# Performance work log

Hardware: AMD Instinct MI355X
Metric: run time of the kernel (lower is better)

## Reference

```python
import jax, jax.numpy as jnp
import numpy as np
import math

HEADS = 16
D_MODEL = 1024
HEAD_DIM = D_MODEL // HEADS
B, S = 2, 2048


def setup_inputs() -> dict:
    key = jax.random.key(0)
    ks = jax.random.split(key, 12)
    sc = 1.0 / math.sqrt(D_MODEL)
    inp = {
        "query": jax.random.normal(ks[0], (B, S, D_MODEL), jnp.float32),
        "key_t": jax.random.normal(ks[1], (B, S, D_MODEL), jnp.float32),
        "value": jax.random.normal(ks[2], (B, S, D_MODEL), jnp.float32),
        "mask": jax.random.randint(ks[3], (B, 1, 1, S), 0, 2, jnp.int32),
        "Wq": jax.random.normal(ks[4], (D_MODEL, D_MODEL), jnp.float32) * sc,
        "bq": jnp.zeros((D_MODEL,), jnp.float32),
        "Wk": jax.random.normal(ks[5], (D_MODEL, D_MODEL), jnp.float32) * sc,
        "bk": jnp.zeros((D_MODEL,), jnp.float32),
        "Wv": jax.random.normal(ks[6], (D_MODEL, D_MODEL), jnp.float32) * sc,
        "bv": jnp.zeros((D_MODEL,), jnp.float32),
        "Wo": jax.random.normal(ks[7], (D_MODEL, D_MODEL), jnp.float32) * sc,
        "bo": jnp.zeros((D_MODEL,), jnp.float32),
    }
    return inp


def _split_heads(x):
    # [B, S, D] -> [B, H, S, Dh]
    b, s, _ = x.shape
    return x.reshape(b, s, HEADS, HEAD_DIM).transpose(0, 2, 1, 3)


def reference(query, key_t, value, mask, Wq, bq, Wk, bk, Wv, bv, Wo, bo):
    # Linear projections (torch Linear: x @ W.T + b)
    q = _split_heads(query @ Wq.T + bq)
    k = _split_heads(key_t @ Wk.T + bk)
    v = _split_heads(value @ Wv.T + bv)
    # Scaled dot-product attention; scale by sqrt(head_dim) = query.size(-1) after split
    scores = jnp.einsum("bhqd,bhkd->bhqk", q, k) / math.sqrt(HEAD_DIM)
    scores = jnp.where(mask == 0, jnp.float32(-1e9), scores)
    prob = jax.nn.softmax(scores, axis=-1)
    # dropout is identity at inference
    attn = jnp.einsum("bhqk,bhkd->bhqd", prob, v)
    # [B, H, S, Dh] -> [B, S, D]
    attn = attn.transpose(0, 2, 1, 3).reshape(query.shape[0], -1, D_MODEL)
    return attn @ Wo.T + bo
```

## Files before the change

kernel.cpp:

```cpp
#include <hip/hip_runtime.h>
#include <hip/hip_bf16.h>

typedef __bf16 bf16;
typedef __bf16 bf16x8 __attribute__((ext_vector_type(8)));
typedef __bf16 bf16x4 __attribute__((ext_vector_type(4)));
typedef float  f32x4  __attribute__((ext_vector_type(4)));
typedef float  f32x16 __attribute__((ext_vector_type(16)));

#define AS1 __attribute__((address_space(1)))
#define AS3 __attribute__((address_space(3)))

__device__ __forceinline__ void gload_lds16(const bf16* g, bf16* l) {
    __builtin_amdgcn_global_load_lds((const AS1 unsigned int*)g,
                                     (AS3 unsigned int*)l, 16, 0, 0);
}

__global__ __launch_bounds__(256) void cast7_k(
    const float* __restrict__ s0, const float* __restrict__ s1,
    const float* __restrict__ s2, const float* __restrict__ s3,
    const float* __restrict__ s4, const float* __restrict__ s5,
    const float* __restrict__ s6,
    bf16* __restrict__ d0, bf16* __restrict__ d1, bf16* __restrict__ d2,
    bf16* __restrict__ d3, bf16* __restrict__ d4, bf16* __restrict__ d5,
    bf16* __restrict__ d6, int n_big, int n_small) {
    int z = blockIdx.z;
    const float* s = (z == 0) ? s0 : (z == 1) ? s1 : (z == 2) ? s2
                   : (z == 3) ? s3 : (z == 4) ? s4 : (z == 5) ? s5 : s6;
    bf16* d = (z == 0) ? d0 : (z == 1) ? d1 : (z == 2) ? d2
            : (z == 3) ? d3 : (z == 4) ? d4 : (z == 5) ? d5 : d6;
    int n = (z < 3) ? n_big : n_small;
    int i = (blockIdx.x * 256 + threadIdx.x) * 8;
    if (i >= n) return;
    float4 a = *(const float4*)(s + i);
    float4 b = *(const float4*)(s + i + 4);
    bf16x8 o;
    o[0] = (bf16)a.x; o[1] = (bf16)a.y; o[2] = (bf16)a.z; o[3] = (bf16)a.w;
    o[4] = (bf16)b.x; o[5] = (bf16)b.y; o[6] = (bf16)b.z; o[7] = (bf16)b.w;
    *(bf16x8*)(d + i) = o;
}

__global__ __launch_bounds__(256) void mask_bias_k(
    const int* __restrict__ m, float* __restrict__ mb, int n) {
    int i = blockIdx.x * 256 + threadIdx.x;
    if (i < n) mb[i] = (m[i] == 0) ? -1.442695e9f : -17.3123405f;
}

template <typename OUT_T, bool TRANS>
__device__ __forceinline__ void gemm32_core(
    const bf16* __restrict__ A, const bf16* __restrict__ W,
    const float* __restrict__ bias, OUT_T* __restrict__ C,
    int M, int N, int K) {
    __shared__ bf16 Asm[128 * 64];
    __shared__ bf16 Bsm[128 * 64];
    const int lane = threadIdx.x & 63;
    const int w = threadIdx.x >> 6;
    const int l31 = lane & 31;
    const int h = lane >> 5;
    const int x7 = l31 & 7;
    const int m0 = blockIdx.x * 128;
    const int n0 = blockIdx.y * 128;
    const int srow = lane >> 3;
    const int scol = ((lane & 7) ^ srow) * 8;
    const int wm = (w & 1) * 64;
    const int wn = (w >> 1) * 64;

    f32x16 acc[2][2] = {};

    for (int k0 = 0; k0 < K; k0 += 64) {
#pragma unroll
        for (int c = 0; c < 4; ++c) {
            int r = w * 32 + c * 8;
            gload_lds16(A + (size_t)(m0 + r + srow) * K + k0 + scol, &Asm[r * 64]);
            gload_lds16(W + (size_t)(n0 + r + srow) * K + k0 + scol, &Bsm[r * 64]);
        }
        __syncthreads();
#pragma unroll
        for (int step = 0; step < 4; ++step) {
            bf16x8 af[2], bfv[2];
#pragma unroll
            for (int i = 0; i < 2; ++i)
                af[i] = *(const bf16x8*)&Asm[(wm + i * 32 + l31) * 64 +
                                             (((step * 2 + h) ^ x7) * 8)];
#pragma unroll
            for (int j = 0; j < 2; ++j)
                bfv[j] = *(const bf16x8*)&Bsm[(wn + j * 32 + l31) * 64 +
                                              (((step * 2 + h) ^ x7) * 8)];
#pragma unroll
            for (int i = 0; i < 2; ++i)
#pragma unroll
                for (int j = 0; j < 2; ++j)
                    acc[i][j] = TRANS
                        ? __builtin_amdgcn_mfma_f32_32x32x16_bf16(bfv[j], af[i],
                                                                  acc[i][j], 0, 0, 0)
                        : __builtin_amdgcn_mfma_f32_32x32x16_bf16(af[i], bfv[j],
                                                                  acc[i][j], 0, 0, 0);
        }
        __syncthreads();
    }
    if (!TRANS) {
#pragma unroll
        for (int i = 0; i < 2; ++i)
#pragma unroll
            for (int j = 0; j < 2; ++j) {
                int col = n0 + wn + j * 32 + l31;
                float bv = bias[col];
#pragma unroll
                for (int g = 0; g < 4; ++g)
#pragma unroll
                    for (int rr = 0; rr < 4; ++rr) {
                        int row = m0 + wm + i * 32 + rr + g * 8 + 4 * h;
                        C[(size_t)row * N + col] =
                            (OUT_T)(acc[i][j][g * 4 + rr] + bv);
                    }
            }
    } else {
#pragma unroll
        for (int i = 0; i < 2; ++i) {
            int s = m0 + wm + i * 32 + l31;
            int b = s >> 11;
            int sl = s & 2047;
            int sp = (sl & ~12) | ((sl & 4) << 1) | ((sl & 8) >> 1);
#pragma unroll
            for (int j = 0; j < 2; ++j)
#pragma unroll
                for (int g = 0; g < 4; ++g) {
                    float4 bv4 = *(const float4*)&bias[n0 + wn + j * 32 + g * 8 + 4 * h];
#pragma unroll
                    for (int rr = 0; rr < 4; ++rr) {
                        int n = n0 + wn + j * 32 + g * 8 + 4 * h + rr;
                        C[(size_t)(b * 1024 + n) * 2048 + sp] =
                            (OUT_T)(acc[i][j][g * 4 + rr] + (&bv4.x)[rr]);
                    }
                }
        }
    }
}

__global__ __launch_bounds__(256) void gemm_qkv(
    const bf16* __restrict__ qb, const bf16* __restrict__ kb, const bf16* __restrict__ vb,
    const bf16* __restrict__ Wq, const bf16* __restrict__ Wk, const bf16* __restrict__ Wv,
    const float* __restrict__ bq, const float* __restrict__ bk, const float* __restrict__ bv,
    bf16* __restrict__ Qp, bf16* __restrict__ Kp, bf16* __restrict__ VpT) {
    int z = blockIdx.z;
    if (z == 2) {
        gemm32_core<bf16, true>(vb, Wv, bv, VpT, 4096, 1024, 1024);
    } else {
        const bf16* A = (z == 0) ? qb : kb;
        const bf16* W = (z == 0) ? Wq : Wk;
        const float* bi = (z == 0) ? bq : bk;
        bf16* C = (z == 0) ? Qp : Kp;
        gemm32_core<bf16, false>(A, W, bi, C, 4096, 1024, 1024);
    }
}

__global__ __launch_bounds__(256) void gemm_out(
    const bf16* __restrict__ A, const bf16* __restrict__ W,
    const float* __restrict__ bias, float* __restrict__ C) {
    gemm32_core<float, false>(A, W, bias, C, 4096, 1024, 1024);
}

__global__ __launch_bounds__(256) void attn_k(
    const bf16* __restrict__ Qp, const bf16* __restrict__ Kp,
    const bf16* __restrict__ VpT, const float* __restrict__ mb,
    bf16* __restrict__ Ao) {
    __shared__ bf16 Ksm[64 * 64];
    __shared__ bf16 Vsm[64 * 64];
    const int q0 = blockIdx.x * 128;
    const int bh = blockIdx.y;
    const int b = bh >> 4, hh = bh & 15;
    const int lane = threadIdx.x & 63, w = threadIdx.x >> 6;
    const int l31 = lane & 31, h = lane >> 5;
    const int x7 = l31 & 7;
    const int srow = lane >> 3, scol = ((lane & 7) ^ srow) * 8;
    const float SC = 0.125f * 1.44269504f;

    const bf16* Qbase =
        Qp + (size_t)(b * 2048 + q0 + w * 32 + l31) * 1024 + hh * 64;
    bf16x8 qf[4];
#pragma unroll
    for (int step = 0; step < 4; ++step)
        qf[step] = *(const bf16x8*)(Qbase + step * 16 + h * 8);

    f32x16 o[2] = {};
    float lsum = 0.0f;

    const float* mbb = mb + b * 2048;
    const bf16* Kg = Kp + (size_t)(b * 2048) * 1024 + hh * 64;
    const bf16* Vg = VpT + (size_t)bh * 64 * 2048;

    for (int k0 = 0; k0 < 2048; k0 += 64) {
#pragma unroll
        for (int c = 0; c < 2; ++c) {
            int r = w * 16 + c * 8;
            gload_lds16(Kg + (size_t)(k0 + r + srow) * 1024 + scol, &Ksm[r * 64]);
            gload_lds16(Vg + (size_t)(r + srow) * 2048 + k0 + scol, &Vsm[r * 64]);
        }
        __syncthreads();

        bf16x8 pa[4];
#pragma unroll
        for (int kg = 0; kg < 2; ++kg) {
            f32x16 z = {};
#pragma unroll
            for (int step = 0; step < 4; ++step) {
                bf16x8 kf = *(const bf16x8*)&Ksm[(kg * 32 + l31) * 64 +
                                                 (((step * 2 + h) ^ x7) * 8)];
                z = __builtin_amdgcn_mfma_f32_32x32x16_bf16(kf, qf[step], z, 0, 0, 0);
            }
            float p[16];
#pragma unroll
            for (int g = 0; g < 4; ++g) {
                float4 bia = *(const float4*)&mbb[k0 + kg * 32 + g * 8 + 4 * h];
                p[g * 4 + 0] = __builtin_amdgcn_exp2f(fmaf(z[g * 4 + 0], SC, bia.x));
                p[g * 4 + 1] = __builtin_amdgcn_exp2f(fmaf(z[g * 4 + 1], SC, bia.y));
                p[g * 4 + 2] = __builtin_amdgcn_exp2f(fmaf(z[g * 4 + 2], SC, bia.z));
                p[g * 4 + 3] = __builtin_amdgcn_exp2f(fmaf(z[g * 4 + 3], SC, bia.w));
            }
#pragma unroll
            for (int t = 0; t < 16; ++t) lsum += p[t];
#pragma unroll
            for (int half = 0; half < 2; ++half) {
                bf16x8 pt;
#pragma unroll
                for (int j = 0; j < 8; ++j) pt[j] = (bf16)p[half * 8 + j];
                pa[kg * 2 + half] = pt;
            }
        }
#pragma unroll
        for (int t = 0; t < 2; ++t)
#pragma unroll
            for (int kk = 0; kk < 4; ++kk) {
                bf16x8 vf = *(const bf16x8*)&Vsm[(t * 32 + l31) * 64 +
                                                 (((kk * 2 + h) ^ x7) * 8)];
                o[t] = __builtin_amdgcn_mfma_f32_32x32x16_bf16(pa[kk], vf, o[t], 0, 0, 0);
            }
        __syncthreads();
    }
    lsum += __shfl_xor(lsum, 32, 64);
    float inv = 1.0f / lsum;
    float ir[16];
#pragma unroll
    for (int g = 0; g < 4; ++g)
#pragma unroll
        for (int rr = 0; rr < 4; ++rr)
            ir[g * 4 + rr] = __shfl(inv, rr + g * 8 + 4 * h, 64);
    const int qbase = b * 2048 + q0 + w * 32;
#pragma unroll
    for (int t = 0; t < 2; ++t)
#pragma unroll
        for (int g = 0; g < 4; ++g)
#pragma unroll
            for (int rr = 0; rr < 4; ++rr) {
                int row = qbase + rr + g * 8 + 4 * h;
                Ao[(size_t)row * 1024 + hh * 64 + t * 32 + l31] =
                    (bf16)(o[t][g * 4 + rr] * ir[g * 4 + rr]);
            }
}

extern "C" void kernel_launch(void* const* d_in, const int* in_sizes, int n_in,
                              void* d_out, int out_size, void* d_ws, size_t ws_size,
                              hipStream_t stream) {
    const float* q   = (const float*)d_in[0];
    const float* kt  = (const float*)d_in[1];
    const float* v   = (const float*)d_in[2];
    const int* mask  = (const int*)d_in[3];
    const float* Wq  = (const float*)d_in[4];
    const float* bq  = (const float*)d_in[5];
    const float* Wk  = (const float*)d_in[6];
    const float* bk  = (const float*)d_in[7];
    const float* Wv  = (const float*)d_in[8];
    const float* bv  = (const float*)d_in[9];
    const float* Wo  = (const float*)d_in[10];
    const float* bo  = (const float*)d_in[11];
    float* out = (float*)d_out;

    char* ws = (char*)d_ws;
    const size_t SZ_IN = 4096ull * 1024 * 2;
    const size_t SZ_W  = 1024ull * 1024 * 2;
    bf16* qb  = (bf16*)(ws + 0 * SZ_IN);
    bf16* kb  = (bf16*)(ws + 1 * SZ_IN);
    bf16* vb  = (bf16*)(ws + 2 * SZ_IN);
    bf16* Wqb = (bf16*)(ws + 3 * SZ_IN);
    bf16* Wkb = (bf16*)(ws + 3 * SZ_IN + 1 * SZ_W);
    bf16* Wvb = (bf16*)(ws + 3 * SZ_IN + 2 * SZ_W);
    bf16* Wob = (bf16*)(ws + 3 * SZ_IN + 3 * SZ_W);
    bf16* Qp  = (bf16*)(ws + 3 * SZ_IN + 4 * SZ_W);
    bf16* Kp  = (bf16*)(ws + 4 * SZ_IN + 4 * SZ_W);
    bf16* VpT = (bf16*)(ws + 5 * SZ_IN + 4 * SZ_W);
    float* mb = (float*)(ws + 6 * SZ_IN + 4 * SZ_W);
    bf16* Ao  = qb;

    const int NIN = 4096 * 1024, NW = 1024 * 1024;
    cast7_k<<<dim3(NIN / 2048, 1, 7), 256, 0, stream>>>(
        q, kt, v, Wq, Wk, Wv, Wo, qb, kb, vb, Wqb, Wkb, Wvb, Wob, NIN, NW);
    mask_bias_k<<<16, 256, 0, stream>>>(mask, mb, 4096);

    gemm_qkv<<<dim3(32, 8, 3), 256, 0, stream>>>(qb, kb, vb, Wqb, Wkb, Wvb,
                                                 bq, bk, bv, Qp, Kp, VpT);
    attn_k<<<dim3(16, 32), 256, 0, stream>>>(Qp, Kp, VpT, mb, Ao);
    gemm_out<<<dim3(32, 8), 256, 0, stream>>>(Ao, Wob, bo, out);
}
```

Measured before the change: 240.3 us.

## Split attention over key ranges with double-buffered KV and halve output GEMM tile

The attention kernel now splits the key dimension into four chunks across blockIdx.z. Each block processes 256 queries (two 32-row groups per wave) and double-buffers K/V tiles in LDS. Unnormalized partial outputs and row sums go to a workspace, and a new combine kernel sums and normalizes them. The output GEMM uses 64-row M tiles to double its block count. This raises parallelism and overlaps loads with compute, at the cost of extra partial-output traffic, an extra launch, and bf16 rounding of partials.

```diff
diff --git a/kernel.cpp b/kernel.cpp
--- a/kernel.cpp
+++ b/kernel.cpp
@@ -45,40 +45,45 @@
     if (i < n) mb[i] = (m[i] == 0) ? -1.442695e9f : -17.3123405f;
 }
 
-template <typename OUT_T, bool TRANS>
+template <typename OUT_T, bool TRANS, int MT>
 __device__ __forceinline__ void gemm32_core(
     const bf16* __restrict__ A, const bf16* __restrict__ W,
     const float* __restrict__ bias, OUT_T* __restrict__ C,
     int M, int N, int K) {
-    __shared__ bf16 Asm[128 * 64];
+    constexpr int MI = MT / 64;
+    __shared__ bf16 Asm[MT * 64];
     __shared__ bf16 Bsm[128 * 64];
     const int lane = threadIdx.x & 63;
     const int w = threadIdx.x >> 6;
     const int l31 = lane & 31;
     const int h = lane >> 5;
     const int x7 = l31 & 7;
-    const int m0 = blockIdx.x * 128;
+    const int m0 = blockIdx.x * MT;
     const int n0 = blockIdx.y * 128;
     const int srow = lane >> 3;
     const int scol = ((lane & 7) ^ srow) * 8;
-    const int wm = (w & 1) * 64;
+    const int wm = (w & 1) * (MT / 2);
     const int wn = (w >> 1) * 64;
 
-    f32x16 acc[2][2] = {};
+    f32x16 acc[MI][2] = {};
 
     for (int k0 = 0; k0 < K; k0 += 64) {
+#pragma unroll
+        for (int c = 0; c < MT / 32; ++c) {
+            int r = w * (MT / 4) + c * 8;
+            gload_lds16(A + (size_t)(m0 + r + srow) * K + k0 + scol, &Asm[r * 64]);
+        }
 #pragma unroll
         for (int c = 0; c < 4; ++c) {
             int r = w * 32 + c * 8;
-            gload_lds16(A + (size_t)(m0 + r + srow) * K + k0 + scol, &Asm[r * 64]);
             gload_lds16(W + (size_t)(n0 + r + srow) * K + k0 + scol, &Bsm[r * 64]);
         }
         __syncthreads();
 #pragma unroll
         for (int step = 0; step < 4; ++step) {
-            bf16x8 af[2], bfv[2];
-#pragma unroll
-            for (int i = 0; i < 2; ++i)
+            bf16x8 af[MI], bfv[2];
+#pragma unroll
+            for (int i = 0; i < MI; ++i)
                 af[i] = *(const bf16x8*)&Asm[(wm + i * 32 + l31) * 64 +
                                              (((step * 2 + h) ^ x7) * 8)];
 #pragma unroll
@@ -86,7 +91,7 @@
                 bfv[j] = *(const bf16x8*)&Bsm[(wn + j * 32 + l31) * 64 +
                                               (((step * 2 + h) ^ x7) * 8)];
 #pragma unroll
-            for (int i = 0; i < 2; ++i)
+            for (int i = 0; i < MI; ++i)
 #pragma unroll
                 for (int j = 0; j < 2; ++j)
                     acc[i][j] = TRANS
@@ -99,7 +104,7 @@
     }
     if (!TRANS) {
 #pragma unroll
-        for (int i = 0; i < 2; ++i)
+        for (int i = 0; i < MI; ++i)
 #pragma unroll
             for (int j = 0; j < 2; ++j) {
                 int col = n0 + wn + j * 32 + l31;
@@ -115,7 +120,7 @@
             }
     } else {
 #pragma unroll
-        for (int i = 0; i < 2; ++i) {
+        for (int i = 0; i < MI; ++i) {
             int s = m0 + wm + i * 32 + l31;
             int b = s >> 11;
             int sl = s & 2047;
@@ -143,118 +148,159 @@
     bf16* __restrict__ Qp, bf16* __restrict__ Kp, bf16* __restrict__ VpT) {
     int z = blockIdx.z;
     if (z == 2) {
-        gemm32_core<bf16, true>(vb, Wv, bv, VpT, 4096, 1024, 1024);
+        gemm32_core<bf16, true, 128>(vb, Wv, bv, VpT, 4096, 1024, 1024);
     } else {
         const bf16* A = (z == 0) ? qb : kb;
         const bf16* W = (z == 0) ? Wq : Wk;
         const float* bi = (z == 0) ? bq : bk;
         bf16* C = (z == 0) ? Qp : Kp;
-        gemm32_core<bf16, false>(A, W, bi, C, 4096, 1024, 1024);
+        gemm32_core<bf16, false, 128>(A, W, bi, C, 4096, 1024, 1024);
     }
 }
 
 __global__ __launch_bounds__(256) void gemm_out(
     const bf16* __restrict__ A, const bf16* __restrict__ W,
     const float* __restrict__ bias, float* __restrict__ C) {
-    gemm32_core<float, false>(A, W, bias, C, 4096, 1024, 1024);
-}
-
-__global__ __launch_bounds__(256) void attn_k(
+    gemm32_core<float, false, 64>(A, W, bias, C, 4096, 1024, 1024);
+}
+
+__global__ __launch_bounds__(256, 2) void attn_k(
     const bf16* __restrict__ Qp, const bf16* __restrict__ Kp,
     const bf16* __restrict__ VpT, const float* __restrict__ mb,
-    bf16* __restrict__ Ao) {
-    __shared__ bf16 Ksm[64 * 64];
-    __shared__ bf16 Vsm[64 * 64];
-    const int q0 = blockIdx.x * 128;
+    bf16* __restrict__ Opart, float* __restrict__ Lpart) {
+    __shared__ bf16 KV[2][2][64 * 64];
+    const int qb = blockIdx.x;
     const int bh = blockIdx.y;
+    const int sp = blockIdx.z;
     const int b = bh >> 4, hh = bh & 15;
     const int lane = threadIdx.x & 63, w = threadIdx.x >> 6;
     const int l31 = lane & 31, h = lane >> 5;
     const int x7 = l31 & 7;
     const int srow = lane >> 3, scol = ((lane & 7) ^ srow) * 8;
     const float SC = 0.125f * 1.44269504f;
-
-    const bf16* Qbase =
-        Qp + (size_t)(b * 2048 + q0 + w * 32 + l31) * 1024 + hh * 64;
-    bf16x8 qf[4];
-#pragma unroll
-    for (int step = 0; step < 4; ++step)
-        qf[step] = *(const bf16x8*)(Qbase + step * 16 + h * 8);
-
-    f32x16 o[2] = {};
-    float lsum = 0.0f;
-
-    const float* mbb = mb + b * 2048;
+    const int q0 = qb * 256;
+    const int k0 = sp * 512;
+
     const bf16* Kg = Kp + (size_t)(b * 2048) * 1024 + hh * 64;
     const bf16* Vg = VpT + (size_t)bh * 64 * 2048;
-
-    for (int k0 = 0; k0 < 2048; k0 += 64) {
+    const float* mbb = mb + b * 2048;
+
+    auto stage = [&](int buf, int kt) {
 #pragma unroll
         for (int c = 0; c < 2; ++c) {
             int r = w * 16 + c * 8;
-            gload_lds16(Kg + (size_t)(k0 + r + srow) * 1024 + scol, &Ksm[r * 64]);
-            gload_lds16(Vg + (size_t)(r + srow) * 2048 + k0 + scol, &Vsm[r * 64]);
-        }
+            gload_lds16(Kg + (size_t)(kt + r + srow) * 1024 + scol,
+                        &KV[buf][0][r * 64]);
+            gload_lds16(Vg + (size_t)(r + srow) * 2048 + kt + scol,
+                        &KV[buf][1][r * 64]);
+        }
+    };
+    stage(0, k0);
+
+    bf16x8 qf[2][4];
+#pragma unroll
+    for (int qg = 0; qg < 2; ++qg) {
+        const bf16* Qbase =
+            Qp + (size_t)(b * 2048 + q0 + w * 64 + qg * 32 + l31) * 1024 + hh * 64;
+#pragma unroll
+        for (int step = 0; step < 4; ++step)
+            qf[qg][step] = *(const bf16x8*)(Qbase + step * 16 + h * 8);
+    }
+
+    f32x16 o[2][2] = {};
+    float lsum[2] = {0.0f, 0.0f};
+
+    for (int it = 0; it < 8; ++it) {
         __syncthreads();
-
-        bf16x8 pa[4];
+        if (it < 7) stage((it + 1) & 1, k0 + (it + 1) * 64);
+        const bf16* Ks = KV[it & 1][0];
+        const bf16* Vs = KV[it & 1][1];
+        const int kt = k0 + it * 64;
+
+        bf16x8 pa[2][4];
 #pragma unroll
         for (int kg = 0; kg < 2; ++kg) {
-            f32x16 z = {};
+            f32x16 z0 = {}, z1 = {};
 #pragma unroll
             for (int step = 0; step < 4; ++step) {
-                bf16x8 kf = *(const bf16x8*)&Ksm[(kg * 32 + l31) * 64 +
-                                                 (((step * 2 + h) ^ x7) * 8)];
-                z = __builtin_amdgcn_mfma_f32_32x32x16_bf16(kf, qf[step], z, 0, 0, 0);
+                bf16x8 kf = *(const bf16x8*)&Ks[(kg * 32 + l31) * 64 +
+                                                (((step * 2 + h) ^ x7) * 8)];
+                z0 = __builtin_amdgcn_mfma_f32_32x32x16_bf16(kf, qf[0][step], z0, 0, 0, 0);
+                z1 = __builtin_amdgcn_mfma_f32_32x32x16_bf16(kf, qf[1][step], z1, 0, 0, 0);
             }
-            float p[16];
 #pragma unroll
             for (int g = 0; g < 4; ++g) {
-                float4 bia = *(const float4*)&mbb[k0 + kg * 32 + g * 8 + 4 * h];
-                p[g * 4 + 0] = __builtin_amdgcn_exp2f(fmaf(z[g * 4 + 0], SC, bia.x));
-                p[g * 4 + 1] = __builtin_amdgcn_exp2f(fmaf(z[g * 4 + 1], SC, bia.y));
-                p[g * 4 + 2] = __builtin_amdgcn_exp2f(fmaf(z[g * 4 + 2], SC, bia.z));
-                p[g * 4 + 3] = __builtin_amdgcn_exp2f(fmaf(z[g * 4 + 3], SC, bia.w));
+                float4 bia = *(const float4*)&mbb[kt + kg * 32 + g * 8 + 4 * h];
+#pragma unroll
+                for (int qg = 0; qg < 2; ++qg) {
+                    const f32x16& z = qg ? z1 : z0;
+                    float p0 = __builtin_amdgcn_exp2f(fmaf(z[g * 4 + 0], SC, bia.x));
+                    float p1 = __builtin_amdgcn_exp2f(fmaf(z[g * 4 + 1], SC, bia.y));
+                    float p2 = __builtin_amdgcn_exp2f(fmaf(z[g * 4 + 2], SC, bia.z));
+                    float p3 = __builtin_amdgcn_exp2f(fmaf(z[g * 4 + 3], SC, bia.w));
+                    lsum[qg] += (p0 + p1) + (p2 + p3);
+                    bf16x8& pf = pa[qg][kg * 2 + (g >> 1)];
+                    int jb = (g & 1) * 4;
+                    pf[jb + 0] = (bf16)p0;
+                    pf[jb + 1] = (bf16)p1;
+                    pf[jb + 2] = (bf16)p2;
+                    pf[jb + 3] = (bf16)p3;
+                }
             }
-#pragma unroll
-            for (int t = 0; t < 16; ++t) lsum += p[t];
-#pragma unroll
-            for (int half = 0; half < 2; ++half) {
-                bf16x8 pt;
-#pragma unroll
-                for (int j = 0; j < 8; ++j) pt[j] = (bf16)p[half * 8 + j];
-                pa[kg * 2 + half] = pt;
+        }
+#pragma unroll
+        for (int t = 0; t < 2; ++t)
+#pragma unroll
+            for (int kk = 0; kk < 4; ++kk) {
+                bf16x8 vf = *(const bf16x8*)&Vs[(t * 32 + l31) * 64 +
+                                                (((kk * 2 + h) ^ x7) * 8)];
+                o[0][t] = __builtin_amdgcn_mfma_f32_32x32x16_bf16(pa[0][kk], vf, o[0][t], 0, 0, 0);
+                o[1][t] = __builtin_amdgcn_mfma_f32_32x32x16_bf16(pa[1][kk], vf, o[1][t], 0, 0, 0);
             }
-        }
+    }
+
+    const size_t pbase = (size_t)(sp * 32 + bh) * 2048;
+#pragma unroll
+    for (int qg = 0; qg < 2; ++qg) {
+        float ls = lsum[qg] + __shfl_xor(lsum[qg], 32, 64);
+        if (h == 0)
+            Lpart[pbase + q0 + w * 64 + qg * 32 + l31] = ls;
 #pragma unroll
         for (int t = 0; t < 2; ++t)
 #pragma unroll
-            for (int kk = 0; kk < 4; ++kk) {
-                bf16x8 vf = *(const bf16x8*)&Vsm[(t * 32 + l31) * 64 +
-                                                 (((kk * 2 + h) ^ x7) * 8)];
-                o[t] = __builtin_amdgcn_mfma_f32_32x32x16_bf16(pa[kk], vf, o[t], 0, 0, 0);
-            }
-        __syncthreads();
-    }
-    lsum += __shfl_xor(lsum, 32, 64);
-    float inv = 1.0f / lsum;
-    float ir[16];
-#pragma unroll
-    for (int g = 0; g < 4; ++g)
-#pragma unroll
-        for (int rr = 0; rr < 4; ++rr)
-            ir[g * 4 + rr] = __shfl(inv, rr + g * 8 + 4 * h, 64);
-    const int qbase = b * 2048 + q0 + w * 32;
-#pragma unroll
-    for (int t = 0; t < 2; ++t)
-#pragma unroll
-        for (int g = 0; g < 4; ++g)
-#pragma unroll
-            for (int rr = 0; rr < 4; ++rr) {
-                int row = qbase + rr + g * 8 + 4 * h;
-                Ao[(size_t)row * 1024 + hh * 64 + t * 32 + l31] =
-                    (bf16)(o[t][g * 4 + rr] * ir[g * 4 + rr]);
-            }
+            for (int g = 0; g < 4; ++g)
+#pragma unroll
+                for (int rr = 0; rr < 4; ++rr) {
+                    int q = q0 + w * 64 + qg * 32 + rr + g * 8 + 4 * h;
+                    Opart[(pbase + q) * 64 + t * 32 + l31] =
+                        (bf16)o[qg][t][g * 4 + rr];
+                }
+    }
+}
+
+__global__ __launch_bounds__(256) void combine_k(
+    const bf16* __restrict__ Op, const float* __restrict__ Lp,
+    bf16* __restrict__ Ao) {
+    int idx = blockIdx.x * 256 + threadIdx.x;
+    int d8 = idx & 7;
+    int q = (idx >> 3) & 2047;
+    int bh = idx >> 14;
+    float acc[8] = {};
+    float l = 0.0f;
+#pragma unroll
+    for (int sp = 0; sp < 4; ++sp) {
+        size_t base = (size_t)(sp * 32 + bh) * 2048 + q;
+        bf16x8 v = *(const bf16x8*)&Op[base * 64 + d8 * 8];
+        l += Lp[base];
+#pragma unroll
+        for (int i = 0; i < 8; ++i) acc[i] += (float)v[i];
+    }
+    float inv = 1.0f / l;
+    bf16x8 ov;
+#pragma unroll
+    for (int i = 0; i < 8; ++i) ov[i] = (bf16)(acc[i] * inv);
+    int b = bh >> 4, hh = bh & 15;
+    *(bf16x8*)&Ao[(size_t)(b * 2048 + q) * 1024 + hh * 64 + d8 * 8] = ov;
 }
 
 extern "C" void kernel_launch(void* const* d_in, const int* in_sizes, int n_in,
@@ -288,6 +334,9 @@
     bf16* Kp  = (bf16*)(ws + 4 * SZ_IN + 4 * SZ_W);
     bf16* VpT = (bf16*)(ws + 5 * SZ_IN + 4 * SZ_W);
     float* mb = (float*)(ws + 6 * SZ_IN + 4 * SZ_W);
+    char*  p0 = ws + 6 * SZ_IN + 4 * SZ_W + (1 << 20);
+    bf16* Opart = (bf16*)p0;
+    float* Lpart = (float*)(p0 + 4ull * 32 * 2048 * 64 * 2);
     bf16* Ao  = qb;
 
     const int NIN = 4096 * 1024, NW = 1024 * 1024;
@@ -297,6 +346,7 @@
 
     gemm_qkv<<<dim3(32, 8, 3), 256, 0, stream>>>(qb, kb, vb, Wqb, Wkb, Wvb,
                                                  bq, bk, bv, Qp, Kp, VpT);
-    attn_k<<<dim3(16, 32), 256, 0, stream>>>(Qp, Kp, VpT, mb, Ao);
-    gemm_out<<<dim3(32, 8), 256, 0, stream>>>(Ao, Wob, bo, out);
-}
+    attn_k<<<dim3(8, 32, 4), 256, 0, stream>>>(Qp, Kp, VpT, mb, Opart, Lpart);
+    combine_k<<<2048, 256, 0, stream>>>(Opart, Lpart, Ao);
+    gemm_out<<<dim3(64, 8), 256, 0, stream>>>(Ao, Wob, bo, out);
+}
```

Result: faster. 228.5 us (-4.9%).
